# Kernel optimization log

Hardware: AMD Instinct MI355X
Metric: run time of the kernel (lower is better)

The kernel has to match this reference:

```python
import jax, jax.numpy as jnp
import numpy as np

HEAD_DIM = 16

def setup_inputs() -> dict:
    key = jax.random.key(0)
    ks = jax.random.split(key, 9)
    dim = 256
    B, H, W = 8, 32, 32
    x  = jax.random.normal(ks[0], (B, H, W, dim), jnp.float32)
    # Conv2d weights in OIHW layout (torch convention), small init
    w3 = jax.random.normal(ks[1], (dim, dim, 1, 1), jnp.float32) * 0.05
    b3 = jax.random.normal(ks[2], (dim,), jnp.float32) * 0.01
    w5 = jax.random.normal(ks[3], (dim, dim, 3, 3), jnp.float32) * 0.02
    b5 = jax.random.normal(ks[4], (dim,), jnp.float32) * 0.01
    w7 = jax.random.normal(ks[5], (dim, dim, 5, 5), jnp.float32) * 0.01
    b7 = jax.random.normal(ks[6], (dim,), jnp.float32) * 0.01
    # nn.Linear weight: (out_features=dim, in_features=attention_dim=dim), no bias
    wp = jax.random.normal(ks[7], (dim, dim), jnp.float32) * 0.05
    return {"x": x, "w3": w3, "b3": b3, "w5": w5, "b5": b5, "w7": w7, "b7": b7, "wp": wp}

def _conv2d_same(x_nchw, w_oihw, b):
    y = jax.lax.conv_general_dilated(
        x_nchw, w_oihw, window_strides=(1, 1), padding='SAME',
        dimension_numbers=('NCHW', 'OIHW', 'NCHW'))
    return y + b[None, :, None, None]

def reference(x, w3, b3, w5, b5, w7, b7, wp):
    B, H, W, C = x.shape
    N = H * W
    nh = C // HEAD_DIM            # num_heads
    scale = HEAD_DIM ** (-0.5)
    xc = jnp.transpose(x, (0, 3, 1, 2))  # NCHW
    # q: 1x1 conv, v: 3x3 conv, k: 5x5 conv (names match the torch code)
    q = _conv2d_same(xc, w3, b3).reshape(B, nh, N, HEAD_DIM)
    v = _conv2d_same(xc, w5, b5).reshape(B, nh, N, HEAD_DIM)
    k = _conv2d_same(xc, w7, b7).reshape(B, nh, N, HEAD_DIM)
    attn = jax.nn.softmax(jnp.einsum('bhnd,bhmd->bhnm', q, k) * scale, axis=-1)
    out = jnp.einsum('bhnm,bhmd->bhnd', attn, v)        # [B, nh, N, hd]
    out = jnp.transpose(out, (0, 2, 1, 3)).reshape(B, H, W, nh * HEAD_DIM)
    return out @ wp.T                                   # Linear, no bias
```

## Files before the change

kernel.cpp:

```cpp
#include <hip/hip_runtime.h>
#include <hip/hip_bf16.h>

#define DIM 256
#define HW  1024

typedef __attribute__((ext_vector_type(8))) short short8;
typedef __attribute__((ext_vector_type(4))) float floatx4;
typedef __attribute__((ext_vector_type(16))) float floatx16;
typedef __attribute__((address_space(1))) const unsigned int g_u32;
typedef __attribute__((address_space(3))) unsigned int l_u32;

#define QSCALE 0.36067376022224085f

__device__ inline unsigned short f2bf(float f) {
  union { float f; unsigned u; } v;
  v.f = f;
  unsigned u = v.u;
  u += 0x7fffu + ((u >> 16) & 1u);
  return (unsigned short)(u >> 16);
}

__device__ inline unsigned short f2bf_trunc(float f) {
  union { float f; unsigned u; } v;
  v.f = f;
  return (unsigned short)(v.u >> 16);
}

__global__ void detect_kernel(const unsigned short* __restrict__ xr,
                              int* __restrict__ flag) {
  __shared__ int cnt;
  if (threadIdx.x == 0) cnt = 0;
  __syncthreads();
  int local = 0;
  for (int i = threadIdx.x; i < 8192; i += 256) {
    unsigned short u = xr[i];
    if ((u & 0x7F80u) == 0x7F80u) local++;
  }
  if (local) atomicAdd(&cnt, local);
  __syncthreads();
  if (threadIdx.x == 0) *flag = (cnt > 0) ? 1 : 0;
}

__device__ inline float ldin(const void* p, long i, int isf32) {
  if (isf32) return ((const float*)p)[i];
  union { unsigned u; float f; } v;
  v.u = ((unsigned)((const unsigned short*)p)[i]) << 16;
  return v.f;
}

__global__ __launch_bounds__(256) void xconv_kernel(
    const void* __restrict__ x, unsigned short* __restrict__ xbf,
    const int* __restrict__ flag) {
  const int isf32 = *flag;
  const int i = (blockIdx.x * 256 + threadIdx.x) * 4;
  if (isf32) {
    const float4 v = *(const float4*)((const float*)x + i);
    ushort4 o;
    o.x = f2bf(v.x); o.y = f2bf(v.y); o.z = f2bf(v.z); o.w = f2bf(v.w);
    *(ushort4*)(xbf + i) = o;
  } else {
    *(ushort4*)(xbf + i) = *(const ushort4*)((const unsigned short*)x + i);
  }
}

__device__ inline void frag_repack2(const void* __restrict__ w,
                                    unsigned short* __restrict__ wF, int KK,
                                    int slice, float* __restrict__ Wl,
                                    int isf32) {
  const int t = threadIdx.x;
  const int co16 = slice & 15;
  const int c8   = slice >> 4;
  const int RE = 32 * KK;
  for (int r = 0; r < 16; ++r) {
    const long base = ((long)((co16 * 16 + r) * 256 + c8 * 32)) * KK;
    for (int i = t; i < RE; i += 256) Wl[r * RE + i] = ldin(w, base + i, isf32);
  }
  __syncthreads();
  for (int tap = 0; tap < KK; ++tap) {
    unsigned short* dst = wF + ((((tap << 3) + c8) << 4) + co16) * 512;
    for (int i = t; i < 512; i += 256) {
      const int lane = i >> 3, j = i & 7;
      const int col = lane & 15;
      const int cis = ((lane >> 4) << 3) + j;
      dst[i] = f2bf(Wl[(col * 32 + cis) * KK + tap]);
    }
  }
}

__global__ __launch_bounds__(256) void wrepack_kernel(
    const void* __restrict__ w3, const void* __restrict__ b3,
    const void* __restrict__ w5, const void* __restrict__ b5,
    const void* __restrict__ w7, const void* __restrict__ b7,
    const void* __restrict__ wp,
    unsigned short* __restrict__ wF3, unsigned short* __restrict__ wF5,
    unsigned short* __restrict__ wF7, unsigned short* __restrict__ wpF,
    float* __restrict__ bc, const int* __restrict__ flag) {
  __shared__ float Wl[12800];
  const int isf32 = *flag;
  const int bid = blockIdx.x;
  const int t = threadIdx.x;
  if (bid < 128) {
    frag_repack2(w7, wF7, 25, bid, Wl, isf32);
  } else if (bid < 256) {
    frag_repack2(w5, wF5, 9, bid - 128, Wl, isf32);
  } else if (bid < 384) {
    frag_repack2(w3, wF3, 1, bid - 256, Wl, isf32);
  } else if (bid < 512) {
    frag_repack2(wp, wpF, 1, bid - 384, Wl, isf32);
  } else {
#pragma unroll
    for (int r = 0; r < 3; ++r) {
      const int i = r * 256 + t;
      const void* src = (i < 256) ? b3 : (i < 512) ? b5 : b7;
      bc[i] = ldin(src, i & 255, isf32);
    }
  }
}

__global__ __launch_bounds__(256, 2) void convqkv_kernel(
    const unsigned short* __restrict__ xbf,
    const unsigned short* __restrict__ wFq,
    const unsigned short* __restrict__ wFv,
    const unsigned short* __restrict__ wFk,
    const float* __restrict__ bc,
    unsigned short* __restrict__ qOut,
    unsigned short* __restrict__ vOut,
    unsigned short* __restrict__ kOut) {
  constexpr int WC = 36;
  constexpr int CELLS = 12 * WC;
  constexpr int LOADS = CELLS * 4;
  __shared__ unsigned short Xs[CELLS * 40];
  __shared__ unsigned short Bs[36 * 512];
  const int t    = threadIdx.x;
  const int bid  = blockIdx.x;
  const int cog0 = bid & 15;
  const int co0  = cog0 << 4;
  const int m0   = (bid >> 4) << 8;
  const int b    = m0 >> 10;
  const int n0   = m0 & 1023;
  const int r0   = n0 >> 5;
  const int wv   = t >> 6;
  const int lane = t & 63;
  const int l15  = lane & 15;
  const int quad = lane >> 4;

  floatx4 aq[4] = {}, av[4] = {}, ak[4] = {};

  for (int c8 = 0; c8 < 8; ++c8) {
    uint4 xreg[7];
#pragma unroll
    for (int rr = 0; rr < 7; ++rr) {
      const int id = rr * 256 + t;
      const int cell = id >> 2, part = id & 3;
      const int hr = cell / WC, wc = cell - hr * WC;
      const int xr = r0 + hr - 2, xc = wc - 2;
      const bool ok = (id < LOADS) && ((unsigned)xr < 32u) &&
                      ((unsigned)xc < 32u);
      const int cr = xr < 0 ? 0 : (xr > 31 ? 31 : xr);
      const int cc = xc < 0 ? 0 : (xc > 31 ? 31 : xc);
      uint4 v = *(const uint4*)&xbf[(((b * 32 + cr) * 32 + cc) << 8) +
                                    (c8 << 5) + (part << 3)];
      if (!ok) v = make_uint4(0, 0, 0, 0);
      xreg[rr] = v;
    }
    __syncthreads();
#pragma unroll
    for (int rr = 0; rr < 9; ++rr) {
      const int tap = (rr << 2) + wv;
      if (tap < 35) {
        const unsigned short* src;
        if (tap < 25) {
          src = &wFk[((((tap << 3) + c8) << 4) + cog0) * 512];
        } else if (tap < 34) {
          src = &wFv[(((((tap - 25) << 3) + c8) << 4) + cog0) * 512];
        } else {
          src = &wFq[((c8 << 4) + cog0) * 512];
        }
        __builtin_amdgcn_global_load_lds((g_u32*)(src + (lane << 3)),
                                         (l_u32*)&Bs[tap << 9], 16, 0, 0);
      }
    }
#pragma unroll
    for (int rr = 0; rr < 7; ++rr) {
      const int id = rr * 256 + t;
      if (id < LOADS)
        *(uint4*)&Xs[(id >> 2) * 40 + ((id & 3) << 3)] = xreg[rr];
    }
    __syncthreads();

#pragma unroll
    for (int tap = 0; tap < 25; ++tap) {
      const int kh = tap / 5, kw = tap % 5;
      const bool vv = (kh >= 1 && kh <= 3 && kw >= 1 && kw <= 3);
      short8 a[4];
#pragma unroll
      for (int rr2 = 0; rr2 < 2; ++rr2) {
#pragma unroll
        for (int ch = 0; ch < 2; ++ch) {
          const unsigned short* xs =
              &Xs[(((wv << 1) + rr2 + kh) * WC + (ch << 4) + l15 + kw) * 40 +
                  (quad << 3)];
          a[(rr2 << 1) + ch] = *(const short8*)xs;
        }
      }
      const short8 kb = *(const short8*)&Bs[(tap << 9) + (lane << 3)];
#pragma unroll
      for (int f = 0; f < 4; ++f)
        ak[f] = __builtin_amdgcn_mfma_f32_16x16x32_bf16(a[f], kb, ak[f],
                                                        0, 0, 0);
      if (vv) {
        const int vt = (kh - 1) * 3 + (kw - 1);
        const short8 vb = *(const short8*)&Bs[((25 + vt) << 9) + (lane << 3)];
#pragma unroll
        for (int f = 0; f < 4; ++f)
          av[f] = __builtin_amdgcn_mfma_f32_16x16x32_bf16(a[f], vb, av[f],
                                                          0, 0, 0);
      }
      if (tap == 12) {
        const short8 qb = *(const short8*)&Bs[(34 << 9) + (lane << 3)];
#pragma unroll
        for (int f = 0; f < 4; ++f)
          aq[f] = __builtin_amdgcn_mfma_f32_16x16x32_bf16(a[f], qb, aq[f],
                                                          0, 0, 0);
      }
    }
  }
#pragma unroll
  for (int rr2 = 0; rr2 < 2; ++rr2) {
#pragma unroll
    for (int ch = 0; ch < 2; ++ch) {
      const int f = (rr2 << 1) + ch;
      const int co = co0 + l15;
      const int slab = (b << 4) + (co >> 4);
      const int clo = co & 15;
      const int nb = n0 + (wv << 6) + (rr2 << 5) + (ch << 4) + (quad << 2);
      {
        const float bj = bc[co];
        floatx4 a = aq[f];
        ushort4 pk4;
        pk4.x = f2bf((a[0] + bj) * QSCALE);
        pk4.y = f2bf((a[1] + bj) * QSCALE);
        pk4.z = f2bf((a[2] + bj) * QSCALE);
        pk4.w = f2bf((a[3] + bj) * QSCALE);
        *(ushort4*)&qOut[(slab << 14) + (clo << 10) + nb] = pk4;
      }
      {
        const float bj = bc[512 + co];
        floatx4 a = ak[f];
        ushort4 pk4;
        pk4.x = f2bf(a[0] + bj); pk4.y = f2bf(a[1] + bj);
        pk4.z = f2bf(a[2] + bj); pk4.w = f2bf(a[3] + bj);
        *(ushort4*)&kOut[(slab << 14) + (clo << 10) + nb] = pk4;
      }
      {
        const float bj = bc[256 + co];
        floatx4 a = av[f];
        const int base = (slab << 14) + (clo << 6);
#pragma unroll
        for (int i = 0; i < 4; ++i) {
          const int n = nb + i;
          vOut[base + ((n & 15) << 10) + (n >> 4)] = f2bf(a[i] + bj);
        }
      }
    }
  }
}

__global__ __launch_bounds__(256, 4) void attn_mfma_kernel(
    const unsigned short* __restrict__ qg,
    const unsigned short* __restrict__ kg,
    const unsigned short* __restrict__ vg,
    unsigned short* __restrict__ out2) {
  __shared__ __align__(16) unsigned short Pb[4][32][40];
  const int t    = threadIdx.x;
  const int w    = t >> 6;
  const int lane = t & 63;
  const int slab = blockIdx.x >> 3;
  const int rb   = blockIdx.x & 7;
  const int b = slab >> 4;
  const int h = slab & 15;
  const int l31  = lane & 31;
  const int hl   = lane >> 5;
  const int l15  = lane & 15;
  const int quad = lane >> 4;

  const unsigned short* Kb = kg + (slab << 14);
  const unsigned short* Vb = vg + (slab << 14);

  const int row0 = (rb << 7) + (w << 5);
  const short8 qa =
      *(const short8*)&qg[(slab << 14) + ((row0 + l31) << 4) + (hl << 3)];

  const short onebf = (short)0x3F80;
  const short8 ones = {onebf, onebf, onebf, onebf, onebf, onebf, onebf, onebf};

  floatx4 acco[2] = {}, asum[2] = {};

  for (int kc = 0; kc < 1024; kc += 32) {
    const short8 kb = *(const short8*)&Kb[((kc + l31) << 4) + (hl << 3)];
    floatx16 s = {};
    s = __builtin_amdgcn_mfma_f32_32x32x16_bf16(qa, kb, s, 0, 0, 0);
#pragma unroll
    for (int r = 0; r < 16; ++r) {
      const float e = __builtin_amdgcn_exp2f(s[r]);
      const int row = (r & 3) + ((r >> 2) << 3) + (hl << 2);
      Pb[w][row][l31] = f2bf_trunc(e);
    }
    const short8 vb = *(const short8*)&Vb[(l15 << 10) + kc + (quad << 3)];
#pragma unroll
    for (int tt = 0; tt < 2; ++tt) {
      const short8 pa = *(const short8*)&Pb[w][(tt << 4) + l15][quad << 3];
      acco[tt] =
          __builtin_amdgcn_mfma_f32_16x16x32_bf16(pa, vb, acco[tt], 0, 0, 0);
      asum[tt] =
          __builtin_amdgcn_mfma_f32_16x16x32_bf16(pa, ones, asum[tt], 0, 0, 0);
    }
  }
#pragma unroll
  for (int tt = 0; tt < 2; ++tt) {
#pragma unroll
    for (int r = 0; r < 4; ++r) {
      const int nloc = (tt << 4) + (quad << 2) + r;
      const float val = acco[tt][r] / asum[tt][r];
      const int n = row0 + nloc;
      out2[(((b << 10) + n) << 8) + (h << 4) + l15] = f2bf(val);
    }
  }
}

__global__ __launch_bounds__(256) void linear_mfma_kernel(
    const unsigned short* __restrict__ inp,
    const unsigned short* __restrict__ wpF,
    void* __restrict__ out, const int* __restrict__ flag) {
  __shared__ unsigned short As[64 * 40];
  const int isf32 = *flag;
  const int t   = threadIdx.x;
  const int m0  = blockIdx.x << 6;
  const int co0 = blockIdx.y << 6;
  const int wv   = t >> 6;
  const int lane = t & 63;
  const int wm = (wv & 1) << 5;
  const int wn = (wv >> 1) << 5;
  const int l15  = lane & 15;
  const int quad = lane >> 4;
  const int cogb = (co0 >> 4) + (wn >> 4);
  const int rowS = t >> 2;
  const int partS = t & 3;

  floatx4 acc[2][2] = {};

  short8 cb0, cb1;
  {
    const unsigned short* wptr = &wpF[(cogb << 9) + (lane << 3)];
    cb0 = *(const short8*)wptr;
    cb1 = *(const short8*)(wptr + 512);
  }
  for (int c8 = 0; c8 < 8; ++c8) {
    const uint4 v = *(const uint4*)&inp[((m0 + rowS) << 8) + (c8 << 5) +
                                        (partS << 3)];
    short8 nb0 = {}, nb1 = {};
    if (c8 + 1 < 8) {
      const unsigned short* wptr =
          &wpF[((((c8 + 1) << 4) + cogb) << 9) + (lane << 3)];
      nb0 = *(const short8*)wptr;
      nb1 = *(const short8*)(wptr + 512);
    }
    __syncthreads();
    *(uint4*)&As[rowS * 40 + (partS << 3)] = v;
    __syncthreads();
    const unsigned short* xs = &As[(wm + l15) * 40 + (quad << 3)];
    const short8 afr0 = *(const short8*)xs;
    const short8 afr1 = *(const short8*)(xs + 16 * 40);
    acc[0][0] = __builtin_amdgcn_mfma_f32_16x16x32_bf16(afr0, cb0,
                                                        acc[0][0], 0, 0, 0);
    acc[0][1] = __builtin_amdgcn_mfma_f32_16x16x32_bf16(afr0, cb1,
                                                        acc[0][1], 0, 0, 0);
    acc[1][0] = __builtin_amdgcn_mfma_f32_16x16x32_bf16(afr1, cb0,
                                                        acc[1][0], 0, 0, 0);
    acc[1][1] = __builtin_amdgcn_mfma_f32_16x16x32_bf16(afr1, cb1,
                                                        acc[1][1], 0, 0, 0);
    cb0 = nb0; cb1 = nb1;
  }
#pragma unroll
  for (int mi = 0; mi < 2; ++mi) {
#pragma unroll
    for (int ni = 0; ni < 2; ++ni) {
      const int co = co0 + wn + (ni << 4) + l15;
      const int mb = m0 + wm + (mi << 4) + (quad << 2);
      floatx4 a = acc[mi][ni];
      if (!isf32) {
        unsigned short* o16 = (unsigned short*)out;
#pragma unroll
        for (int r = 0; r < 4; ++r) o16[(mb + r) * 256 + co] = f2bf(a[r]);
      } else {
        float* o32 = (float*)out;
#pragma unroll
        for (int r = 0; r < 4; ++r) o32[(mb + r) * 256 + co] = a[r];
      }
    }
  }
}

extern "C" void kernel_launch(void* const* d_in, const int* in_sizes, int n_in,
                              void* d_out, int out_size, void* d_ws,
                              size_t ws_size, hipStream_t stream) {
  const void* x  = d_in[0];
  const void* w3 = d_in[1];
  const void* b3 = d_in[2];
  const void* w5 = d_in[3];
  const void* b5 = d_in[4];
  const void* w7 = d_in[5];
  const void* b7 = d_in[6];
  const void* wp = d_in[7];

  char* p = (char*)d_ws;
  int* flag = (int*)p;                       p += 256;
  unsigned short* xbf = (unsigned short*)p;  p += 4u * 1024 * 1024;
  unsigned short* wF3 = (unsigned short*)p;  p += 131072;
  unsigned short* wF5 = (unsigned short*)p;  p += 1179648;
  unsigned short* wF7 = (unsigned short*)p;  p += 3276800;
  unsigned short* wpF = (unsigned short*)p;  p += 131072;
  float* bc = (float*)p;                     p += 4096;
  unsigned short* qc  = (unsigned short*)p;  p += 4194304;
  unsigned short* kT  = (unsigned short*)p;  p += 4194304;
  unsigned short* vT  = (unsigned short*)p;  p += 4194304;
  unsigned short* o2b = (unsigned short*)p;  p += 4194304;

  detect_kernel<<<1, 256, 0, stream>>>((const unsigned short*)x, flag);

  xconv_kernel<<<2048, 256, 0, stream>>>(x, xbf, flag);
  wrepack_kernel<<<513, 256, 0, stream>>>(w3, b3, w5, b5, w7, b7, wp, wF3,
                                          wF5, wF7, wpF, bc, flag);

  convqkv_kernel<<<512, 256, 0, stream>>>(xbf, wF3, wF5, wF7, bc, qc, vT, kT);

  attn_mfma_kernel<<<1024, 256, 0, stream>>>(qc, kT, vT, o2b);

  dim3 lg(128, 4);
  linear_mfma_kernel<<<lg, 256, 0, stream>>>(o2b, wpF, d_out, flag);
}
```

Before: 179.5 us.

## Widen convqkv tiles to two output-channel groups per block

Each conv block now computes 32 output channels instead of 16, so every staged input-patch fragment read from LDS feeds two MFMAs per tap. The grid halves to 256 blocks and the weight staging buffer roughly doubles. The aim is to halve the redundant input loads and LDS A-fragment reads across channel groups. In exchange, accumulator registers double and launch bounds drop to one block per CU, and 256 blocks on a 256-CU part leaves little latency hiding.

```diff
diff --git a/kernel.cpp b/kernel.cpp
--- a/kernel.cpp
+++ b/kernel.cpp
@@ -117,7 +117,7 @@
   }
 }
 
-__global__ __launch_bounds__(256, 2) void convqkv_kernel(
+__global__ __launch_bounds__(256, 1) void convqkv_kernel(
     const unsigned short* __restrict__ xbf,
     const unsigned short* __restrict__ wFq,
     const unsigned short* __restrict__ wFv,
@@ -130,12 +130,12 @@
   constexpr int CELLS = 12 * WC;
   constexpr int LOADS = CELLS * 4;
   __shared__ unsigned short Xs[CELLS * 40];
-  __shared__ unsigned short Bs[36 * 512];
+  __shared__ unsigned short Bs[70 * 512];
   const int t    = threadIdx.x;
   const int bid  = blockIdx.x;
-  const int cog0 = bid & 15;
+  const int cog0 = (bid & 7) << 1;
   const int co0  = cog0 << 4;
-  const int m0   = (bid >> 4) << 8;
+  const int m0   = (bid >> 3) << 8;
   const int b    = m0 >> 10;
   const int n0   = m0 & 1023;
   const int r0   = n0 >> 5;
@@ -144,7 +144,7 @@
   const int l15  = lane & 15;
   const int quad = lane >> 4;
 
-  floatx4 aq[4] = {}, av[4] = {}, ak[4] = {};
+  floatx4 aq[4][2] = {}, av[4][2] = {}, ak[4][2] = {};
 
   for (int c8 = 0; c8 < 8; ++c8) {
     uint4 xreg[7];
@@ -165,19 +165,20 @@
     }
     __syncthreads();
 #pragma unroll
-    for (int rr = 0; rr < 9; ++rr) {
-      const int tap = (rr << 2) + wv;
-      if (tap < 35) {
+    for (int rr = 0; rr < 18; ++rr) {
+      const int slot = (rr << 2) + wv;
+      if (slot < 70) {
+        const int tap = slot >> 1, ni = slot & 1;
         const unsigned short* src;
         if (tap < 25) {
-          src = &wFk[((((tap << 3) + c8) << 4) + cog0) * 512];
+          src = &wFk[((((tap << 3) + c8) << 4) + cog0 + ni) * 512];
         } else if (tap < 34) {
-          src = &wFv[(((((tap - 25) << 3) + c8) << 4) + cog0) * 512];
+          src = &wFv[(((((tap - 25) << 3) + c8) << 4) + cog0 + ni) * 512];
         } else {
-          src = &wFq[((c8 << 4) + cog0) * 512];
+          src = &wFq[((c8 << 4) + cog0 + ni) * 512];
         }
         __builtin_amdgcn_global_load_lds((g_u32*)(src + (lane << 3)),
-                                         (l_u32*)&Bs[tap << 9], 16, 0, 0);
+                                         (l_u32*)&Bs[slot << 9], 16, 0, 0);
       }
     }
 #pragma unroll
@@ -203,25 +204,39 @@
           a[(rr2 << 1) + ch] = *(const short8*)xs;
         }
       }
-      const short8 kb = *(const short8*)&Bs[(tap << 9) + (lane << 3)];
-#pragma unroll
-      for (int f = 0; f < 4; ++f)
-        ak[f] = __builtin_amdgcn_mfma_f32_16x16x32_bf16(a[f], kb, ak[f],
-                                                        0, 0, 0);
+      const short8 kb0 = *(const short8*)&Bs[((tap << 1) << 9) + (lane << 3)];
+      const short8 kb1 =
+          *(const short8*)&Bs[(((tap << 1) + 1) << 9) + (lane << 3)];
+#pragma unroll
+      for (int f = 0; f < 4; ++f) {
+        ak[f][0] = __builtin_amdgcn_mfma_f32_16x16x32_bf16(a[f], kb0,
+                                                           ak[f][0], 0, 0, 0);
+        ak[f][1] = __builtin_amdgcn_mfma_f32_16x16x32_bf16(a[f], kb1,
+                                                           ak[f][1], 0, 0, 0);
+      }
       if (vv) {
         const int vt = (kh - 1) * 3 + (kw - 1);
-        const short8 vb = *(const short8*)&Bs[((25 + vt) << 9) + (lane << 3)];
-#pragma unroll
-        for (int f = 0; f < 4; ++f)
-          av[f] = __builtin_amdgcn_mfma_f32_16x16x32_bf16(a[f], vb, av[f],
-                                                          0, 0, 0);
+        const int vs = 50 + (vt << 1);
+        const short8 vb0 = *(const short8*)&Bs[(vs << 9) + (lane << 3)];
+        const short8 vb1 = *(const short8*)&Bs[((vs + 1) << 9) + (lane << 3)];
+#pragma unroll
+        for (int f = 0; f < 4; ++f) {
+          av[f][0] = __builtin_amdgcn_mfma_f32_16x16x32_bf16(a[f], vb0,
+                                                             av[f][0], 0, 0, 0);
+          av[f][1] = __builtin_amdgcn_mfma_f32_16x16x32_bf16(a[f], vb1,
+                                                             av[f][1], 0, 0, 0);
+        }
       }
       if (tap == 12) {
-        const short8 qb = *(const short8*)&Bs[(34 << 9) + (lane << 3)];
-#pragma unroll
-        for (int f = 0; f < 4; ++f)
-          aq[f] = __builtin_amdgcn_mfma_f32_16x16x32_bf16(a[f], qb, aq[f],
-                                                          0, 0, 0);
+        const short8 qb0 = *(const short8*)&Bs[(68 << 9) + (lane << 3)];
+        const short8 qb1 = *(const short8*)&Bs[(69 << 9) + (lane << 3)];
+#pragma unroll
+        for (int f = 0; f < 4; ++f) {
+          aq[f][0] = __builtin_amdgcn_mfma_f32_16x16x32_bf16(a[f], qb0,
+                                                             aq[f][0], 0, 0, 0);
+          aq[f][1] = __builtin_amdgcn_mfma_f32_16x16x32_bf16(a[f], qb1,
+                                                             aq[f][1], 0, 0, 0);
+        }
       }
     }
   }
@@ -230,36 +245,39 @@
 #pragma unroll
     for (int ch = 0; ch < 2; ++ch) {
       const int f = (rr2 << 1) + ch;
-      const int co = co0 + l15;
-      const int slab = (b << 4) + (co >> 4);
-      const int clo = co & 15;
       const int nb = n0 + (wv << 6) + (rr2 << 5) + (ch << 4) + (quad << 2);
-      {
-        const float bj = bc[co];
-        floatx4 a = aq[f];
-        ushort4 pk4;
-        pk4.x = f2bf((a[0] + bj) * QSCALE);
-        pk4.y = f2bf((a[1] + bj) * QSCALE);
-        pk4.z = f2bf((a[2] + bj) * QSCALE);
-        pk4.w = f2bf((a[3] + bj) * QSCALE);
-        *(ushort4*)&qOut[(slab << 14) + (clo << 10) + nb] = pk4;
-      }
-      {
-        const float bj = bc[512 + co];
-        floatx4 a = ak[f];
-        ushort4 pk4;
-        pk4.x = f2bf(a[0] + bj); pk4.y = f2bf(a[1] + bj);
-        pk4.z = f2bf(a[2] + bj); pk4.w = f2bf(a[3] + bj);
-        *(ushort4*)&kOut[(slab << 14) + (clo << 10) + nb] = pk4;
-      }
-      {
-        const float bj = bc[256 + co];
-        floatx4 a = av[f];
-        const int base = (slab << 14) + (clo << 6);
-#pragma unroll
-        for (int i = 0; i < 4; ++i) {
-          const int n = nb + i;
-          vOut[base + ((n & 15) << 10) + (n >> 4)] = f2bf(a[i] + bj);
+#pragma unroll
+      for (int ni = 0; ni < 2; ++ni) {
+        const int co = co0 + (ni << 4) + l15;
+        const int slab = (b << 4) + (co >> 4);
+        const int clo = co & 15;
+        {
+          const float bj = bc[co];
+          floatx4 a = aq[f][ni];
+          ushort4 pk4;
+          pk4.x = f2bf((a[0] + bj) * QSCALE);
+          pk4.y = f2bf((a[1] + bj) * QSCALE);
+          pk4.z = f2bf((a[2] + bj) * QSCALE);
+          pk4.w = f2bf((a[3] + bj) * QSCALE);
+          *(ushort4*)&qOut[(slab << 14) + (clo << 10) + nb] = pk4;
+        }
+        {
+          const float bj = bc[512 + co];
+          floatx4 a = ak[f][ni];
+          ushort4 pk4;
+          pk4.x = f2bf(a[0] + bj); pk4.y = f2bf(a[1] + bj);
+          pk4.z = f2bf(a[2] + bj); pk4.w = f2bf(a[3] + bj);
+          *(ushort4*)&kOut[(slab << 14) + (clo << 10) + nb] = pk4;
+        }
+        {
+          const float bj = bc[256 + co];
+          floatx4 a = av[f][ni];
+          const int base = (slab << 14) + (clo << 6);
+#pragma unroll
+          for (int i = 0; i < 4; ++i) {
+            const int n = nb + i;
+            vOut[base + ((n & 15) << 10) + (n >> 4)] = f2bf(a[i] + bj);
+          }
         }
       }
     }
@@ -432,7 +450,7 @@
   wrepack_kernel<<<513, 256, 0, stream>>>(w3, b3, w5, b5, w7, b7, wp, wF3,
                                           wF5, wF7, wpF, bc, flag);
 
-  convqkv_kernel<<<512, 256, 0, stream>>>(xbf, wF3, wF5, wF7, bc, qc, vT, kT);
+  convqkv_kernel<<<256, 256, 0, stream>>>(xbf, wF3, wF5, wF7, bc, qc, vT, kT);
 
   attn_mfma_kernel<<<1024, 256, 0, stream>>>(qc, kT, vT, o2b);
 
```

New measurement: 189.1 us. 5.4% more time.
